# Performance work log

Measured on AMD Instinct MI355X. Metric: run time of the kernel, lower is better.

Reference implementation:

```python
import jax, jax.numpy as jnp
import numpy as np

HS = 512
IN = 512
FS = 128


def setup_inputs() -> dict:
    key = jax.random.key(0)
    ks = jax.random.split(key, 6)
    stdv = 1.0 / np.sqrt(HS)
    u = lambda k, shape: jax.random.uniform(k, shape, jnp.float32, -stdv, stdv)
    return {
        "word_input": jax.random.normal(ks[0], (128, 512, IN), jnp.float32),
        "field_input": jax.random.normal(ks[1], (128, 512, FS), jnp.float32),
        "W_f": u(ks[2], (IN, 4 * HS)),
        "Wz": u(ks[3], (FS, 2 * HS)),
        "U_f": u(ks[4], (HS, 4 * HS)),
        "bias_f": jnp.zeros((4 * HS,), jnp.float32),
        "biasz": jnp.zeros((2 * HS,), jnp.float32),
    }


def reference(word_input, field_input, W_f, Wz, U_f, bias_f, biasz):
    bs = word_input.shape[0]
    # Precompute input and field projections once (hoisted out of recurrence).
    x_proj = jnp.einsum("bsi,ih->bsh", word_input, W_f) + bias_f   # [B,S,4H]
    fgates = jnp.einsum("bsf,fh->bsh", field_input, Wz) + biasz     # [B,S,2H]
    lt = jax.nn.sigmoid(fgates[..., :HS])
    zt = jnp.tanh(fgates[..., HS:])
    lz = lt * zt                                                    # [B,S,H]

    h0 = jnp.zeros((bs, HS), jnp.float32)
    c0 = jnp.zeros((bs, HS), jnp.float32)

    def step(carry, inp):
        h_t, c_t = carry
        xp_t, lz_t = inp
        gates = xp_t + h_t @ U_f                     # [B,4H]
        i_t = jax.nn.sigmoid(gates[:, :HS])
        f_t = jax.nn.sigmoid(gates[:, HS:2 * HS] + 1.0)
        g_t = jnp.tanh(gates[:, 2 * HS:3 * HS])
        o_t = jax.nn.sigmoid(gates[:, 3 * HS:])
        c_t = f_t * c_t + i_t * g_t + lz_t
        h_t = o_t * jnp.tanh(c_t)
        return (h_t, c_t), h_t

    (h_T, c_T), hs = jax.lax.scan(
        step, (h0, c0),
        (jnp.swapaxes(x_proj, 0, 1), jnp.swapaxes(lz, 0, 1)))  # scan over seq
    hidden_seq = jnp.swapaxes(hs, 0, 1)  # [B,S,H]
    return hidden_seq, (h_T, c_T)
```

## Files before the change

kernel.cpp:

```cpp
#include <hip/hip_runtime.h>
#include <hip/hip_bf16.h>

#define BATCH 128
#define SEQ   512
#define IND   512
#define FSD   128
#define HS    512
#define G4    (4 * HS)
#define G2    (2 * HS)

#define NG 8
#define GB 16
#define NS 32
#define SJ 16

typedef short short8_t __attribute__((ext_vector_type(8)));
typedef float f32x4 __attribute__((ext_vector_type(4)));

static __device__ __forceinline__ unsigned short f2bf(float f) {
    unsigned int u = __float_as_uint(f);
    unsigned int r = (u + 0x7fffu + ((u >> 16) & 1u)) >> 16;
    return (unsigned short)r;
}
static __device__ __forceinline__ float bf2f(unsigned short b) {
    return __uint_as_float(((unsigned int)b) << 16);
}
static __device__ __forceinline__ float sigmoidf_(float x) {
    return 1.0f / (1.0f + __expf(-x));
}

__global__ __launch_bounds__(256)
void uconv_kernel(const float* __restrict__ Uf, unsigned short* __restrict__ Up) {
    int idx = blockIdx.x * 256 + threadIdx.x;
    int i  = idx & 7;
    int l  = (idx >> 3) & 63;
    int kt = (idx >> 9) & 15;
    int g  = (idx >> 13) & 3;
    int s  = idx >> 15;
    int k  = kt * 32 + ((l >> 4) << 3) + i;
    int col = g * 512 + s * 16 + (l & 15);
    Up[idx] = f2bf(Uf[(size_t)k * G4 + col]);
}

__global__ __launch_bounds__(256)
void wtconv_kernel(const float* __restrict__ Wf, unsigned short* __restrict__ WfT) {
    __shared__ float tile[64][65];
    int k0 = blockIdx.x * 64;
    int n0 = blockIdx.y * 64;
    int tid = threadIdx.x;
    int r = tid >> 6, c = tid & 63;
    #pragma unroll
    for (int i = 0; i < 16; ++i)
        tile[r + 4 * i][c] = Wf[(size_t)(k0 + r + 4 * i) * G4 + n0 + c];
    __syncthreads();
    #pragma unroll
    for (int i = 0; i < 16; ++i)
        WfT[(size_t)(n0 + r + 4 * i) * IND + k0 + c] = f2bf(tile[c][r + 4 * i]);
}

__global__ __launch_bounds__(256)
void wzconv_kernel(const float* __restrict__ Wz, unsigned short* __restrict__ WzT) {
    __shared__ float tile[64][65];
    int k0 = blockIdx.x * 64;
    int n0 = blockIdx.y * 64;
    int tid = threadIdx.x;
    int r = tid >> 6, c = tid & 63;
    #pragma unroll
    for (int i = 0; i < 16; ++i)
        tile[r + 4 * i][c] = Wz[(size_t)(k0 + r + 4 * i) * G2 + n0 + c];
    __syncthreads();
    #pragma unroll
    for (int i = 0; i < 16; ++i)
        WzT[(size_t)(n0 + r + 4 * i) * FSD + k0 + c] = f2bf(tile[c][r + 4 * i]);
}

__global__ __launch_bounds__(256)
void lzmm_kernel(const float* __restrict__ field, const unsigned short* __restrict__ WzT,
                 const float* __restrict__ biasz, unsigned short* __restrict__ lzOut) {
    __shared__ unsigned short As[128 * 64];
    __shared__ unsigned short Bs[128 * 64];
    int tid = threadIdx.x;
    int l = tid & 63, w = tid >> 6;
    int wr = w >> 1, wc = w & 1;
    int row0 = blockIdx.x * 128;
    int j0 = blockIdx.y * 64;

    f32x4 acc[4][4];
    #pragma unroll
    for (int m = 0; m < 4; ++m)
        #pragma unroll
        for (int n = 0; n < 4; ++n)
            acc[m][n] = (f32x4){0.f, 0.f, 0.f, 0.f};

    for (int k0 = 0; k0 < FSD; k0 += 64) {
        float4 av[4][2];
        short8_t bv[4];
        #pragma unroll
        for (int i = 0; i < 4; ++i) {
            int cidx = tid + 256 * i;
            int ar = cidx >> 3, sub = cidx & 7;
            int grow = row0 + ar;
            int b_ = grow & 127, s_ = grow >> 7;
            const float* ap = field + ((size_t)b_ * SEQ + s_) * FSD + k0 + sub * 8;
            av[i][0] = *(const float4*)ap;
            av[i][1] = *(const float4*)(ap + 4);
            int wzcol = ((ar >> 4) & 1) * HS + j0 + (((ar >> 5) << 4) | (ar & 15));
            bv[i] = *(const short8_t*)(WzT + (size_t)wzcol * FSD + k0 + sub * 8);
        }
        __syncthreads();
        #pragma unroll
        for (int i = 0; i < 4; ++i) {
            int cidx = tid + 256 * i;
            int ar = cidx >> 3, sub = cidx & 7;
            int off = ar * 64 + ((sub ^ (ar & 7)) << 3);
            short8_t a8;
            a8[0] = (short)f2bf(av[i][0].x); a8[1] = (short)f2bf(av[i][0].y);
            a8[2] = (short)f2bf(av[i][0].z); a8[3] = (short)f2bf(av[i][0].w);
            a8[4] = (short)f2bf(av[i][1].x); a8[5] = (short)f2bf(av[i][1].y);
            a8[6] = (short)f2bf(av[i][1].z); a8[7] = (short)f2bf(av[i][1].w);
            *(short8_t*)&As[off] = a8;
            *(short8_t*)&Bs[off] = bv[i];
        }
        __syncthreads();
        #pragma unroll
        for (int kt = 0; kt < 2; ++kt) {
            short8_t af[4], bfr[4];
            #pragma unroll
            for (int m = 0; m < 4; ++m) {
                int r = wr * 64 + m * 16 + (l & 15);
                int sub = kt * 4 + (l >> 4);
                af[m] = *(const short8_t*)&As[r * 64 + ((sub ^ (r & 7)) << 3)];
                int cc = wc * 64 + m * 16 + (l & 15);
                bfr[m] = *(const short8_t*)&Bs[cc * 64 + ((sub ^ (cc & 7)) << 3)];
            }
            #pragma unroll
            for (int m = 0; m < 4; ++m)
                #pragma unroll
                for (int n = 0; n < 4; ++n)
                    acc[m][n] = __builtin_amdgcn_mfma_f32_16x16x32_bf16(
                        af[m], bfr[n], acc[m][n], 0, 0, 0);
        }
        __syncthreads();
    }
    #pragma unroll
    for (int m = 0; m < 4; ++m) {
        int grow = row0 + wr * 64 + m * 16 + (l >> 4) * 4;
        #pragma unroll
        for (int q = 0; q < 2; ++q) {
            int j = j0 + (wc * 2 + q) * 16 + (l & 15);
            float bl = biasz[j];
            float bz = biasz[HS + j];
            f32x4 al = acc[m][2 * q];
            f32x4 az = acc[m][2 * q + 1];
            #pragma unroll
            for (int r = 0; r < 4; ++r) {
                float lv = sigmoidf_(al[r] + bl);
                float zv = tanhf(az[r] + bz);
                lzOut[(size_t)(grow + r) * HS + j] = f2bf(lv * zv);
            }
        }
    }
}

#define XBM 128
#define XBN 128
#define XBK 64
__global__ __launch_bounds__(256)
void xmm_kernel(const float* __restrict__ word, const unsigned short* __restrict__ WfT,
                const float* __restrict__ bias, unsigned short* __restrict__ xp) {
    __shared__ unsigned short As[XBM * XBK];
    __shared__ unsigned short Bs[XBN * XBK];
    int tid = threadIdx.x;
    int l = tid & 63, w = tid >> 6;
    int wr = w >> 1, wc = w & 1;
    int row0 = blockIdx.x * XBM;
    int col0 = blockIdx.y * XBN;

    f32x4 acc[4][4];
    #pragma unroll
    for (int m = 0; m < 4; ++m)
        #pragma unroll
        for (int n = 0; n < 4; ++n)
            acc[m][n] = (f32x4){0.f, 0.f, 0.f, 0.f};

    for (int k0 = 0; k0 < IND; k0 += XBK) {
        float4 av[4][2];
        short8_t bv[4];
        #pragma unroll
        for (int i = 0; i < 4; ++i) {
            int c = tid + 256 * i;
            int ar = c >> 3, sub = c & 7;
            int grow = row0 + ar;
            int b_ = grow & 127, s_ = grow >> 7;
            const float* ap = word + ((size_t)b_ * SEQ + s_) * IND + k0 + sub * 8;
            av[i][0] = *(const float4*)ap;
            av[i][1] = *(const float4*)(ap + 4);
            bv[i] = *(const short8_t*)(WfT + (size_t)(col0 + ar) * IND + k0 + sub * 8);
        }
        __syncthreads();
        #pragma unroll
        for (int i = 0; i < 4; ++i) {
            int c = tid + 256 * i;
            int ar = c >> 3, sub = c & 7;
            int off = ar * 64 + ((sub ^ (ar & 7)) << 3);
            short8_t a8;
            a8[0] = (short)f2bf(av[i][0].x); a8[1] = (short)f2bf(av[i][0].y);
            a8[2] = (short)f2bf(av[i][0].z); a8[3] = (short)f2bf(av[i][0].w);
            a8[4] = (short)f2bf(av[i][1].x); a8[5] = (short)f2bf(av[i][1].y);
            a8[6] = (short)f2bf(av[i][1].z); a8[7] = (short)f2bf(av[i][1].w);
            *(short8_t*)&As[off] = a8;
            *(short8_t*)&Bs[off] = bv[i];
        }
        __syncthreads();
        #pragma unroll
        for (int kt = 0; kt < 2; ++kt) {
            short8_t af[4], bfr[4];
            #pragma unroll
            for (int m = 0; m < 4; ++m) {
                int r = wr * 64 + m * 16 + (l & 15);
                int sub = kt * 4 + (l >> 4);
                af[m] = *(const short8_t*)&As[r * 64 + ((sub ^ (r & 7)) << 3)];
                int cc = wc * 64 + m * 16 + (l & 15);
                bfr[m] = *(const short8_t*)&Bs[cc * 64 + ((sub ^ (cc & 7)) << 3)];
            }
            #pragma unroll
            for (int m = 0; m < 4; ++m)
                #pragma unroll
                for (int n = 0; n < 4; ++n)
                    acc[m][n] = __builtin_amdgcn_mfma_f32_16x16x32_bf16(
                        af[m], bfr[n], acc[m][n], 0, 0, 0);
        }
    }
    #pragma unroll
    for (int m = 0; m < 4; ++m) {
        int grow = row0 + wr * 64 + m * 16 + (l >> 4) * 4;
        #pragma unroll
        for (int n = 0; n < 4; ++n) {
            int gcol = col0 + wc * 64 + n * 16 + (l & 15);
            float bsv = bias[gcol];
            #pragma unroll
            for (int r = 0; r < 4; ++r)
                xp[(size_t)(grow + r) * G4 + gcol] = f2bf(acc[m][n][r] + bsv);
        }
    }
}

__global__ __launch_bounds__(256, 1)
void rec12_kernel(const unsigned short* __restrict__ xp,
                  const unsigned short* __restrict__ lz,
                  const unsigned short* __restrict__ Up,
                  float* __restrict__ out,
                  unsigned short* __restrict__ hbuf,
                  unsigned int* __restrict__ flags) {
    const size_t HSEQ = (size_t)BATCH * SEQ * HS;
    const int HBG = GB * HS;

    int bid = blockIdx.x;
    int g = bid & 7;
    int s = bid >> 3;
    int tid = threadIdx.x;
    int w = tid >> 6;
    int l = tid & 63;

    __shared__ short8_t Ubs[4][16][64];
    {
        const short8_t* upw = (const short8_t*)(Up + ((size_t)(s * 4 + w) * 16) * 512);
        #pragma unroll
        for (int kt = 0; kt < 16; ++kt)
            Ubs[w][kt][l] = upw[kt * 64 + l];
    }
    __shared__ short8_t ha_lds[16][64];
    __shared__ float gbuf[4][16][18];
    __syncthreads();

    int eb = tid >> 4;
    int ej = tid & 15;
    int jg = s * SJ + ej;
    int bg = g * GB + eb;
    int widx = (((jg >> 5) * 64 + eb + (((jg >> 3) & 3) << 4)) << 3) + (jg & 7);

    unsigned int* fl = flags + (size_t)g * 2 * NS;

    float c = 0.f, h_last = 0.f;

    for (int t = 0; t < SEQ; ++t) {
        size_t xb = ((size_t)t * BATCH + bg) * G4;
        float pgi = bf2f(xp[xb + jg]);
        float pgf = bf2f(xp[xb + HS + jg]);
        float pgg = bf2f(xp[xb + 2 * HS + jg]);
        float pgo = bf2f(xp[xb + 3 * HS + jg]);
        float plz = bf2f(lz[((size_t)t * BATCH + bg) * HS + jg]);

        f32x4 acc0 = {0.f, 0.f, 0.f, 0.f};
        f32x4 acc1 = {0.f, 0.f, 0.f, 0.f};
        if (t > 0) {
            if (w == 0) {
                const unsigned int* fp = fl + ((t - 1) & 1) * NS + (l & 31);
                int spins = 0;
                unsigned v;
                do {
                    v = __hip_atomic_load(fp, __ATOMIC_RELAXED,
                                          __HIP_MEMORY_SCOPE_AGENT);
                    if (++spins > (1 << 20)) break;
                } while (!__all(v == (unsigned)t));

                const unsigned long long* ha64 = (const unsigned long long*)
                    (hbuf + (size_t)(((t - 1) & 1) * NG + g) * HBG);
                unsigned long long A2a[16], A2b[16];
                #pragma unroll
                for (int kt = 0; kt < 16; ++kt) {
                    int i0 = (kt * 64 + l) * 2;
                    A2a[kt] = __hip_atomic_load(&ha64[i0], __ATOMIC_RELAXED,
                                                __HIP_MEMORY_SCOPE_AGENT);
                    A2b[kt] = __hip_atomic_load(&ha64[i0 + 1], __ATOMIC_RELAXED,
                                                __HIP_MEMORY_SCOPE_AGENT);
                }
                #pragma unroll
                for (int kt = 0; kt < 16; ++kt) {
                    union { unsigned long long u[2]; short8_t v8; } A;
                    A.u[0] = A2a[kt]; A.u[1] = A2b[kt];
                    ha_lds[kt][l] = A.v8;
                }
            }
            __syncthreads();

            #pragma unroll
            for (int kt = 0; kt < 16; ++kt) {
                short8_t av = ha_lds[kt][l];
                short8_t bf = Ubs[w][kt][l];
                if (kt & 1)
                    acc1 = __builtin_amdgcn_mfma_f32_16x16x32_bf16(av, bf, acc1, 0, 0, 0);
                else
                    acc0 = __builtin_amdgcn_mfma_f32_16x16x32_bf16(av, bf, acc0, 0, 0, 0);
            }
            acc0 += acc1;
        }
        #pragma unroll
        for (int r = 0; r < 4; ++r)
            gbuf[w][(l >> 4) * 4 + r][l & 15] = acc0[r];
        __syncthreads();

        float gi = gbuf[0][eb][ej] + pgi;
        float gf = gbuf[1][eb][ej] + pgf;
        float gg = gbuf[2][eb][ej] + pgg;
        float go = gbuf[3][eb][ej] + pgo;
        float i_ = sigmoidf_(gi);
        float f_ = sigmoidf_(gf + 1.0f);
        float g_ = tanhf(gg);
        float o_ = sigmoidf_(go);
        c = f_ * c + i_ * g_ + plz;
        float h = o_ * tanhf(c);
        h_last = h;

        unsigned short hv = f2bf(h);
        unsigned partner = (unsigned)(unsigned short)__shfl_down((int)hv, 1);
        if ((ej & 1) == 0) {
            unsigned int* hb32 = (unsigned int*)
                (hbuf + (size_t)((t & 1) * NG + g) * HBG);
            __hip_atomic_store(&hb32[widx >> 1], (unsigned)hv | (partner << 16),
                               __ATOMIC_RELAXED, __HIP_MEMORY_SCOPE_AGENT);
        }
        asm volatile("s_waitcnt vmcnt(0)" ::: "memory");
        __syncthreads();
        if (tid == 0)
            __hip_atomic_store(&fl[(t & 1) * NS + s], (unsigned)(t + 1),
                               __ATOMIC_RELAXED, __HIP_MEMORY_SCOPE_AGENT);

        out[((size_t)bg * SEQ + t) * HS + jg] = h;
    }

    out[HSEQ + (size_t)bg * HS + jg] = h_last;
    out[HSEQ + (size_t)BATCH * HS + (size_t)bg * HS + jg] = c;
}

extern "C" void kernel_launch(void* const* d_in, const int* in_sizes, int n_in,
                              void* d_out, int out_size, void* d_ws, size_t ws_size,
                              hipStream_t stream) {
    const float* word   = (const float*)d_in[0];
    const float* field  = (const float*)d_in[1];
    const float* Wf     = (const float*)d_in[2];
    const float* Wz     = (const float*)d_in[3];
    const float* Uf     = (const float*)d_in[4];
    const float* bias_f = (const float*)d_in[5];
    const float* biasz  = (const float*)d_in[6];
    float* out = (float*)d_out;

    char* p = (char*)d_ws;
    unsigned short* xp   = (unsigned short*)p;  p += (size_t)SEQ * BATCH * G4 * 2;
    unsigned short* lzb  = (unsigned short*)p;  p += (size_t)SEQ * BATCH * HS * 2;
    unsigned short* Up   = (unsigned short*)p;  p += (size_t)IND * G4 * 2;
    unsigned short* WfT  = (unsigned short*)p;  p += (size_t)G4 * IND * 2;
    unsigned short* WzT  = (unsigned short*)p;  p += (size_t)G2 * FSD * 2;
    unsigned short* hbuf = (unsigned short*)p;  p += (size_t)2 * NG * GB * HS * 2;
    unsigned int*   flags= (unsigned int*)p;    p += (size_t)NG * 2 * NS * 4;

    hipMemsetAsync(flags, 0, (size_t)NG * 2 * NS * 4, stream);

    uconv_kernel<<<(IND * G4) / 256, 256, 0, stream>>>(Uf, Up);

    dim3 gt(IND / 64, G4 / 64);
    wtconv_kernel<<<gt, 256, 0, stream>>>(Wf, WfT);

    dim3 gz(FSD / 64, G2 / 64);
    wzconv_kernel<<<gz, 256, 0, stream>>>(Wz, WzT);

    dim3 glz((SEQ * BATCH) / 128, HS / 64);
    lzmm_kernel<<<glz, 256, 0, stream>>>(field, WzT, biasz, lzb);

    dim3 gx((SEQ * BATCH) / XBM, G4 / XBN);
    xmm_kernel<<<gx, 256, 0, stream>>>(word, WfT, bias_f, xp);

    rec12_kernel<<<NG * NS, 256, 0, stream>>>(xp, lzb, Up, out, hbuf, flags);
}
```

Measured before the change: 1.803 ms.

## Halve recurrence workgroups with 32 hidden units each; swizzle GEMM grid per XCD

The recurrent kernel now launches 128 workgroups instead of 256. Each handles 32 hidden columns, with two U-slices held in LDS and two MFMA chains per wave, and each thread updates two batch rows. This halves the number of participants in the per-step flag barrier and the spinning on flags, but doubles the serial MFMA and elementwise work per workgroup on every step. Separately, the input-projection GEMM switches to a 1D grid remapped so that each XCD gets a contiguous band of rows, which is meant to improve L2 locality.

```diff
diff --git a/kernel.cpp b/kernel.cpp
--- a/kernel.cpp
+++ b/kernel.cpp
@@ -11,8 +11,8 @@
 
 #define NG 8
 #define GB 16
-#define NS 32
-#define SJ 16
+#define NB2 16
+#define SJ2 32
 
 typedef short short8_t __attribute__((ext_vector_type(8)));
 typedef float f32x4 __attribute__((ext_vector_type(4)));
@@ -173,8 +173,11 @@
     int tid = threadIdx.x;
     int l = tid & 63, w = tid >> 6;
     int wr = w >> 1, wc = w & 1;
-    int row0 = blockIdx.x * XBM;
-    int col0 = blockIdx.y * XBN;
+    int lin = blockIdx.x;
+    int xcd = lin & 7;
+    int idx = lin >> 3;
+    int col0 = (idx & 15) * XBN;
+    int row0 = (xcd * 64 + (idx >> 4)) * XBM;
 
     f32x4 acc[4][4];
     #pragma unroll
@@ -246,7 +249,7 @@
 }
 
 __global__ __launch_bounds__(256, 1)
-void rec12_kernel(const unsigned short* __restrict__ xp,
+void rec13_kernel(const unsigned short* __restrict__ xp,
                   const unsigned short* __restrict__ lz,
                   const unsigned short* __restrict__ Up,
                   float* __restrict__ out,
@@ -262,40 +265,50 @@
     int w = tid >> 6;
     int l = tid & 63;
 
-    __shared__ short8_t Ubs[4][16][64];
-    {
-        const short8_t* upw = (const short8_t*)(Up + ((size_t)(s * 4 + w) * 16) * 512);
+    __shared__ short8_t Ubs[2][4][16][64];
+    #pragma unroll
+    for (int sl = 0; sl < 2; ++sl) {
+        const short8_t* upw =
+            (const short8_t*)(Up + ((size_t)((2 * s + sl) * 4 + w) * 16) * 512);
         #pragma unroll
         for (int kt = 0; kt < 16; ++kt)
-            Ubs[w][kt][l] = upw[kt * 64 + l];
+            Ubs[sl][w][kt][l] = upw[kt * 64 + l];
     }
     __shared__ short8_t ha_lds[16][64];
-    __shared__ float gbuf[4][16][18];
+    __shared__ float gbuf[4][16][34];
     __syncthreads();
 
-    int eb = tid >> 4;
-    int ej = tid & 15;
-    int jg = s * SJ + ej;
-    int bg = g * GB + eb;
-    int widx = (((jg >> 5) * 64 + eb + (((jg >> 3) & 3) << 4)) << 3) + (jg & 7);
-
-    unsigned int* fl = flags + (size_t)g * 2 * NS;
-
-    float c = 0.f, h_last = 0.f;
+    int ej = tid & 31;
+    int eb0 = tid >> 5;
+    int jg = s * SJ2 + ej;
+    int bg0 = g * GB + eb0;
+    int bg1 = bg0 + 8;
+    int w0 = (((jg >> 5) * 64 + eb0 + (((jg >> 3) & 3) << 4)) << 3) + (jg & 7);
+    int w1 = w0 + 64;
+
+    unsigned int* fl = flags + (size_t)g * 2 * NB2;
+
+    float c0 = 0.f, c1 = 0.f, h0l = 0.f, h1l = 0.f;
 
     for (int t = 0; t < SEQ; ++t) {
-        size_t xb = ((size_t)t * BATCH + bg) * G4;
-        float pgi = bf2f(xp[xb + jg]);
-        float pgf = bf2f(xp[xb + HS + jg]);
-        float pgg = bf2f(xp[xb + 2 * HS + jg]);
-        float pgo = bf2f(xp[xb + 3 * HS + jg]);
-        float plz = bf2f(lz[((size_t)t * BATCH + bg) * HS + jg]);
-
-        f32x4 acc0 = {0.f, 0.f, 0.f, 0.f};
-        f32x4 acc1 = {0.f, 0.f, 0.f, 0.f};
+        size_t xb0 = ((size_t)t * BATCH + bg0) * G4;
+        size_t xb1 = ((size_t)t * BATCH + bg1) * G4;
+        float pgi0 = bf2f(xp[xb0 + jg]);
+        float pgf0 = bf2f(xp[xb0 + HS + jg]);
+        float pgg0 = bf2f(xp[xb0 + 2 * HS + jg]);
+        float pgo0 = bf2f(xp[xb0 + 3 * HS + jg]);
+        float pgi1 = bf2f(xp[xb1 + jg]);
+        float pgf1 = bf2f(xp[xb1 + HS + jg]);
+        float pgg1 = bf2f(xp[xb1 + 2 * HS + jg]);
+        float pgo1 = bf2f(xp[xb1 + 3 * HS + jg]);
+        float plz0 = bf2f(lz[((size_t)t * BATCH + bg0) * HS + jg]);
+        float plz1 = bf2f(lz[((size_t)t * BATCH + bg1) * HS + jg]);
+
+        f32x4 aA0 = {0.f,0.f,0.f,0.f}, aA1 = {0.f,0.f,0.f,0.f};
+        f32x4 aB0 = {0.f,0.f,0.f,0.f}, aB1 = {0.f,0.f,0.f,0.f};
         if (t > 0) {
             if (w == 0) {
-                const unsigned int* fp = fl + ((t - 1) & 1) * NS + (l & 31);
+                const unsigned int* fp = fl + ((t - 1) & 1) * NB2 + (l & 15);
                 int spins = 0;
                 unsigned v;
                 do {
@@ -327,50 +340,69 @@
             #pragma unroll
             for (int kt = 0; kt < 16; ++kt) {
                 short8_t av = ha_lds[kt][l];
-                short8_t bf = Ubs[w][kt][l];
-                if (kt & 1)
-                    acc1 = __builtin_amdgcn_mfma_f32_16x16x32_bf16(av, bf, acc1, 0, 0, 0);
-                else
-                    acc0 = __builtin_amdgcn_mfma_f32_16x16x32_bf16(av, bf, acc0, 0, 0, 0);
+                short8_t bfA = Ubs[0][w][kt][l];
+                short8_t bfB = Ubs[1][w][kt][l];
+                if (kt & 1) {
+                    aA1 = __builtin_amdgcn_mfma_f32_16x16x32_bf16(av, bfA, aA1, 0, 0, 0);
+                    aB1 = __builtin_amdgcn_mfma_f32_16x16x32_bf16(av, bfB, aB1, 0, 0, 0);
+                } else {
+                    aA0 = __builtin_amdgcn_mfma_f32_16x16x32_bf16(av, bfA, aA0, 0, 0, 0);
+                    aB0 = __builtin_amdgcn_mfma_f32_16x16x32_bf16(av, bfB, aB0, 0, 0, 0);
+                }
             }
-            acc0 += acc1;
-        }
-        #pragma unroll
-        for (int r = 0; r < 4; ++r)
-            gbuf[w][(l >> 4) * 4 + r][l & 15] = acc0[r];
-        __syncthreads();
-
-        float gi = gbuf[0][eb][ej] + pgi;
-        float gf = gbuf[1][eb][ej] + pgf;
-        float gg = gbuf[2][eb][ej] + pgg;
-        float go = gbuf[3][eb][ej] + pgo;
-        float i_ = sigmoidf_(gi);
-        float f_ = sigmoidf_(gf + 1.0f);
-        float g_ = tanhf(gg);
-        float o_ = sigmoidf_(go);
-        c = f_ * c + i_ * g_ + plz;
-        float h = o_ * tanhf(c);
-        h_last = h;
-
-        unsigned short hv = f2bf(h);
-        unsigned partner = (unsigned)(unsigned short)__shfl_down((int)hv, 1);
+            aA0 += aA1;
+            aB0 += aB1;
+        }
+        #pragma unroll
+        for (int r = 0; r < 4; ++r) {
+            gbuf[w][(l >> 4) * 4 + r][l & 15] = aA0[r];
+            gbuf[w][(l >> 4) * 4 + r][16 + (l & 15)] = aB0[r];
+        }
+        __syncthreads();
+
+        float gi0 = gbuf[0][eb0][ej] + pgi0;
+        float gf0 = gbuf[1][eb0][ej] + pgf0;
+        float gg0 = gbuf[2][eb0][ej] + pgg0;
+        float go0 = gbuf[3][eb0][ej] + pgo0;
+        float gi1 = gbuf[0][eb0 + 8][ej] + pgi1;
+        float gf1 = gbuf[1][eb0 + 8][ej] + pgf1;
+        float gg1 = gbuf[2][eb0 + 8][ej] + pgg1;
+        float go1 = gbuf[3][eb0 + 8][ej] + pgo1;
+        float i0 = sigmoidf_(gi0), f0 = sigmoidf_(gf0 + 1.0f);
+        float q0 = tanhf(gg0),     o0 = sigmoidf_(go0);
+        float i1 = sigmoidf_(gi1), f1 = sigmoidf_(gf1 + 1.0f);
+        float q1 = tanhf(gg1),     o1 = sigmoidf_(go1);
+        c0 = f0 * c0 + i0 * q0 + plz0;
+        c1 = f1 * c1 + i1 * q1 + plz1;
+        float h0 = o0 * tanhf(c0);
+        float h1 = o1 * tanhf(c1);
+        h0l = h0; h1l = h1;
+
+        unsigned short hv0 = f2bf(h0), hv1 = f2bf(h1);
+        unsigned p0 = (unsigned)(unsigned short)__shfl_down((int)hv0, 1);
+        unsigned p1 = (unsigned)(unsigned short)__shfl_down((int)hv1, 1);
         if ((ej & 1) == 0) {
             unsigned int* hb32 = (unsigned int*)
                 (hbuf + (size_t)((t & 1) * NG + g) * HBG);
-            __hip_atomic_store(&hb32[widx >> 1], (unsigned)hv | (partner << 16),
+            __hip_atomic_store(&hb32[w0 >> 1], (unsigned)hv0 | (p0 << 16),
                                __ATOMIC_RELAXED, __HIP_MEMORY_SCOPE_AGENT);
+            __hip_atomic_store(&hb32[w1 >> 1], (unsigned)hv1 | (p1 << 16),
+                               __ATOMIC_RELAXED, __HIP_MEMORY_SCOPE_AGENT);
         }
         asm volatile("s_waitcnt vmcnt(0)" ::: "memory");
         __syncthreads();
         if (tid == 0)
-            __hip_atomic_store(&fl[(t & 1) * NS + s], (unsigned)(t + 1),
+            __hip_atomic_store(&fl[(t & 1) * NB2 + s], (unsigned)(t + 1),
                                __ATOMIC_RELAXED, __HIP_MEMORY_SCOPE_AGENT);
 
-        out[((size_t)bg * SEQ + t) * HS + jg] = h;
-    }
-
-    out[HSEQ + (size_t)bg * HS + jg] = h_last;
-    out[HSEQ + (size_t)BATCH * HS + (size_t)bg * HS + jg] = c;
+        out[((size_t)bg0 * SEQ + t) * HS + jg] = h0;
+        out[((size_t)bg1 * SEQ + t) * HS + jg] = h1;
+    }
+
+    out[HSEQ + (size_t)bg0 * HS + jg] = h0l;
+    out[HSEQ + (size_t)bg1 * HS + jg] = h1l;
+    out[HSEQ + (size_t)BATCH * HS + (size_t)bg0 * HS + jg] = c0;
+    out[HSEQ + (size_t)BATCH * HS + (size_t)bg1 * HS + jg] = c1;
 }
 
 extern "C" void kernel_launch(void* const* d_in, const int* in_sizes, int n_in,
@@ -392,9 +424,9 @@
     unsigned short* WfT  = (unsigned short*)p;  p += (size_t)G4 * IND * 2;
     unsigned short* WzT  = (unsigned short*)p;  p += (size_t)G2 * FSD * 2;
     unsigned short* hbuf = (unsigned short*)p;  p += (size_t)2 * NG * GB * HS * 2;
-    unsigned int*   flags= (unsigned int*)p;    p += (size_t)NG * 2 * NS * 4;
-
-    hipMemsetAsync(flags, 0, (size_t)NG * 2 * NS * 4, stream);
+    unsigned int*   flags= (unsigned int*)p;    p += 2048;
+
+    hipMemsetAsync(flags, 0, 2048, stream);
 
     uconv_kernel<<<(IND * G4) / 256, 256, 0, stream>>>(Uf, Up);
 
@@ -407,8 +439,8 @@
     dim3 glz((SEQ * BATCH) / 128, HS / 64);
     lzmm_kernel<<<glz, 256, 0, stream>>>(field, WzT, biasz, lzb);
 
-    dim3 gx((SEQ * BATCH) / XBM, G4 / XBN);
-    xmm_kernel<<<gx, 256, 0, stream>>>(word, WfT, bias_f, xp);
-
-    rec12_kernel<<<NG * NS, 256, 0, stream>>>(xp, lzb, Up, out, hbuf, flags);
-}
+    xmm_kernel<<<(SEQ * BATCH / XBM) * (G4 / XBN), 256, 0, stream>>>(
+        word, WfT, bias_f, xp);
+
+    rec13_kernel<<<NG * NB2, 256, 0, stream>>>(xp, lzb, Up, out, hbuf, flags);
+}
```

Result: slower. 1.962 ms (+8.8%).

## Tag hidden-state words with timestep to replace flag barrier in recurrence

Applied to the files above, without the earlier changes.

The recurrent kernel no longer uses separate per-block flags with a store/waitcnt/syncthreads/flag-store handshake. Each h value is stored as a 32-bit word holding the bf16 value plus a timestep tag, and consumers spin directly on the data until every tag matches, with all four waves polling in parallel instead of one. This removes a barrier and a round trip per step on the critical serial path, at the cost of doubling hbuf traffic and adding tag checks. Separately, the input-projection GEMM grid is linearised and remapped so blocks sharing rows land on the same XCD, aiming for better L2 reuse.

```diff
diff --git a/kernel.cpp b/kernel.cpp
--- a/kernel.cpp
+++ b/kernel.cpp
@@ -173,8 +173,11 @@
     int tid = threadIdx.x;
     int l = tid & 63, w = tid >> 6;
     int wr = w >> 1, wc = w & 1;
-    int row0 = blockIdx.x * XBM;
-    int col0 = blockIdx.y * XBN;
+    int lin = blockIdx.x;
+    int xcd = lin & 7;
+    int idx = lin >> 3;
+    int col0 = (idx & 15) * XBN;
+    int row0 = (xcd * 64 + (idx >> 4)) * XBM;
 
     f32x4 acc[4][4];
     #pragma unroll
@@ -246,12 +249,11 @@
 }
 
 __global__ __launch_bounds__(256, 1)
-void rec12_kernel(const unsigned short* __restrict__ xp,
+void rec14_kernel(const unsigned short* __restrict__ xp,
                   const unsigned short* __restrict__ lz,
                   const unsigned short* __restrict__ Up,
                   float* __restrict__ out,
-                  unsigned short* __restrict__ hbuf,
-                  unsigned int* __restrict__ flags) {
+                  unsigned int* __restrict__ hbuf) {
     const size_t HSEQ = (size_t)BATCH * SEQ * HS;
     const int HBG = GB * HS;
 
@@ -278,8 +280,6 @@
     int jg = s * SJ + ej;
     int bg = g * GB + eb;
     int widx = (((jg >> 5) * 64 + eb + (((jg >> 3) & 3) << 4)) << 3) + (jg & 7);
-
-    unsigned int* fl = flags + (size_t)g * 2 * NS;
 
     float c = 0.f, h_last = 0.f;
 
@@ -294,33 +294,41 @@
         f32x4 acc0 = {0.f, 0.f, 0.f, 0.f};
         f32x4 acc1 = {0.f, 0.f, 0.f, 0.f};
         if (t > 0) {
-            if (w == 0) {
-                const unsigned int* fp = fl + ((t - 1) & 1) * NS + (l & 31);
+            unsigned expect = (unsigned)t;
+            const unsigned long long* ha64 = (const unsigned long long*)
+                (hbuf + (size_t)(((t - 1) & 1) * NG + g) * HBG);
+            #pragma unroll
+            for (int q = 0; q < 4; ++q) {
+                int kt = w * 4 + q;
+                const unsigned long long* pk = ha64 + (size_t)kt * 256 + l * 4;
+                unsigned long long x0, x1, x2, x3;
                 int spins = 0;
-                unsigned v;
-                do {
-                    v = __hip_atomic_load(fp, __ATOMIC_RELAXED,
-                                          __HIP_MEMORY_SCOPE_AGENT);
-                    if (++spins > (1 << 20)) break;
-                } while (!__all(v == (unsigned)t));
-
-                const unsigned long long* ha64 = (const unsigned long long*)
-                    (hbuf + (size_t)(((t - 1) & 1) * NG + g) * HBG);
-                unsigned long long A2a[16], A2b[16];
-                #pragma unroll
-                for (int kt = 0; kt < 16; ++kt) {
-                    int i0 = (kt * 64 + l) * 2;
-                    A2a[kt] = __hip_atomic_load(&ha64[i0], __ATOMIC_RELAXED,
-                                                __HIP_MEMORY_SCOPE_AGENT);
-                    A2b[kt] = __hip_atomic_load(&ha64[i0 + 1], __ATOMIC_RELAXED,
-                                                __HIP_MEMORY_SCOPE_AGENT);
+                for (;;) {
+                    x0 = __hip_atomic_load(pk + 0, __ATOMIC_RELAXED,
+                                           __HIP_MEMORY_SCOPE_AGENT);
+                    x1 = __hip_atomic_load(pk + 1, __ATOMIC_RELAXED,
+                                           __HIP_MEMORY_SCOPE_AGENT);
+                    x2 = __hip_atomic_load(pk + 2, __ATOMIC_RELAXED,
+                                           __HIP_MEMORY_SCOPE_AGENT);
+                    x3 = __hip_atomic_load(pk + 3, __ATOMIC_RELAXED,
+                                           __HIP_MEMORY_SCOPE_AGENT);
+                    bool ok =
+                        (((unsigned)(x0 >> 16) & 0xffffu) == expect) &
+                        (((unsigned)(x0 >> 48)) == expect) &
+                        (((unsigned)(x1 >> 16) & 0xffffu) == expect) &
+                        (((unsigned)(x1 >> 48)) == expect) &
+                        (((unsigned)(x2 >> 16) & 0xffffu) == expect) &
+                        (((unsigned)(x2 >> 48)) == expect) &
+                        (((unsigned)(x3 >> 16) & 0xffffu) == expect) &
+                        (((unsigned)(x3 >> 48)) == expect);
+                    if (__all(ok) || ++spins > (1 << 20)) break;
                 }
-                #pragma unroll
-                for (int kt = 0; kt < 16; ++kt) {
-                    union { unsigned long long u[2]; short8_t v8; } A;
-                    A.u[0] = A2a[kt]; A.u[1] = A2b[kt];
-                    ha_lds[kt][l] = A.v8;
-                }
+                union { unsigned int u[4]; short8_t v8; } A;
+                A.u[0] = __builtin_amdgcn_perm((unsigned)(x0 >> 32), (unsigned)x0, 0x05040100u);
+                A.u[1] = __builtin_amdgcn_perm((unsigned)(x1 >> 32), (unsigned)x1, 0x05040100u);
+                A.u[2] = __builtin_amdgcn_perm((unsigned)(x2 >> 32), (unsigned)x2, 0x05040100u);
+                A.u[3] = __builtin_amdgcn_perm((unsigned)(x3 >> 32), (unsigned)x3, 0x05040100u);
+                ha_lds[kt][l] = A.v8;
             }
             __syncthreads();
 
@@ -352,19 +360,10 @@
         float h = o_ * tanhf(c);
         h_last = h;
 
-        unsigned short hv = f2bf(h);
-        unsigned partner = (unsigned)(unsigned short)__shfl_down((int)hv, 1);
-        if ((ej & 1) == 0) {
-            unsigned int* hb32 = (unsigned int*)
-                (hbuf + (size_t)((t & 1) * NG + g) * HBG);
-            __hip_atomic_store(&hb32[widx >> 1], (unsigned)hv | (partner << 16),
-                               __ATOMIC_RELAXED, __HIP_MEMORY_SCOPE_AGENT);
-        }
-        asm volatile("s_waitcnt vmcnt(0)" ::: "memory");
-        __syncthreads();
-        if (tid == 0)
-            __hip_atomic_store(&fl[(t & 1) * NS + s], (unsigned)(t + 1),
-                               __ATOMIC_RELAXED, __HIP_MEMORY_SCOPE_AGENT);
+        unsigned tagval = (unsigned)f2bf(h) | ((unsigned)(t + 1) << 16);
+        unsigned int* hb = hbuf + (size_t)((t & 1) * NG + g) * HBG;
+        __hip_atomic_store(&hb[widx], tagval, __ATOMIC_RELAXED,
+                           __HIP_MEMORY_SCOPE_AGENT);
 
         out[((size_t)bg * SEQ + t) * HS + jg] = h;
     }
@@ -391,10 +390,9 @@
     unsigned short* Up   = (unsigned short*)p;  p += (size_t)IND * G4 * 2;
     unsigned short* WfT  = (unsigned short*)p;  p += (size_t)G4 * IND * 2;
     unsigned short* WzT  = (unsigned short*)p;  p += (size_t)G2 * FSD * 2;
-    unsigned short* hbuf = (unsigned short*)p;  p += (size_t)2 * NG * GB * HS * 2;
-    unsigned int*   flags= (unsigned int*)p;    p += (size_t)NG * 2 * NS * 4;
-
-    hipMemsetAsync(flags, 0, (size_t)NG * 2 * NS * 4, stream);
+    unsigned int*   hbuf = (unsigned int*)p;    p += (size_t)2 * NG * GB * HS * 4;
+
+    hipMemsetAsync(hbuf, 0, (size_t)2 * NG * GB * HS * 4, stream);
 
     uconv_kernel<<<(IND * G4) / 256, 256, 0, stream>>>(Uf, Up);
 
@@ -407,8 +405,8 @@
     dim3 glz((SEQ * BATCH) / 128, HS / 64);
     lzmm_kernel<<<glz, 256, 0, stream>>>(field, WzT, biasz, lzb);
 
-    dim3 gx((SEQ * BATCH) / XBM, G4 / XBN);
-    xmm_kernel<<<gx, 256, 0, stream>>>(word, WfT, bias_f, xp);
-
-    rec12_kernel<<<NG * NS, 256, 0, stream>>>(xp, lzb, Up, out, hbuf, flags);
-}
+    xmm_kernel<<<(SEQ * BATCH / XBM) * (G4 / XBN), 256, 0, stream>>>(
+        word, WfT, bias_f, xp);
+
+    rec14_kernel<<<NG * NS, 256, 0, stream>>>(xp, lzb, Up, out, hbuf);
+}
```

Result: slower. 2.319 ms (+28.6%).

## Use per-wave completion flags in recurrence and XCD-swizzle the input GEMM grid

Applied to the files above, without the earlier changes.

The recurrent kernel drops the block-wide barrier before publishing step completion; each wave now writes its own flag, and waiters poll four times as many flags with two loads per lane. The input-projection GEMM switches to a 1D grid remapped so that blocks on the same XCD share row tiles, improving L2 reuse. The per-wave flags shorten the critical path per timestep but raise polling traffic.

```diff
diff --git a/kernel.cpp b/kernel.cpp
--- a/kernel.cpp
+++ b/kernel.cpp
@@ -173,8 +173,11 @@
     int tid = threadIdx.x;
     int l = tid & 63, w = tid >> 6;
     int wr = w >> 1, wc = w & 1;
-    int row0 = blockIdx.x * XBM;
-    int col0 = blockIdx.y * XBN;
+    int lin = blockIdx.x;
+    int xcd = lin & 7;
+    int idx = lin >> 3;
+    int col0 = (idx & 15) * XBN;
+    int row0 = (xcd * 64 + (idx >> 4)) * XBM;
 
     f32x4 acc[4][4];
     #pragma unroll
@@ -246,7 +249,7 @@
 }
 
 __global__ __launch_bounds__(256, 1)
-void rec12_kernel(const unsigned short* __restrict__ xp,
+void rec15_kernel(const unsigned short* __restrict__ xp,
                   const unsigned short* __restrict__ lz,
                   const unsigned short* __restrict__ Up,
                   float* __restrict__ out,
@@ -279,7 +282,7 @@
     int bg = g * GB + eb;
     int widx = (((jg >> 5) * 64 + eb + (((jg >> 3) & 3) << 4)) << 3) + (jg & 7);
 
-    unsigned int* fl = flags + (size_t)g * 2 * NS;
+    unsigned int* fl = flags + (size_t)g * 2 * NS * 4;
 
     float c = 0.f, h_last = 0.f;
 
@@ -295,14 +298,18 @@
         f32x4 acc1 = {0.f, 0.f, 0.f, 0.f};
         if (t > 0) {
             if (w == 0) {
-                const unsigned int* fp = fl + ((t - 1) & 1) * NS + (l & 31);
+                const unsigned int* fb = fl + ((t - 1) & 1) * NS * 4;
+                const unsigned int* fp0 = fb + l;
+                const unsigned int* fp1 = fb + 64 + l;
                 int spins = 0;
-                unsigned v;
+                unsigned v0, v1;
                 do {
-                    v = __hip_atomic_load(fp, __ATOMIC_RELAXED,
-                                          __HIP_MEMORY_SCOPE_AGENT);
+                    v0 = __hip_atomic_load(fp0, __ATOMIC_RELAXED,
+                                           __HIP_MEMORY_SCOPE_AGENT);
+                    v1 = __hip_atomic_load(fp1, __ATOMIC_RELAXED,
+                                           __HIP_MEMORY_SCOPE_AGENT);
                     if (++spins > (1 << 20)) break;
-                } while (!__all(v == (unsigned)t));
+                } while (!__all((v0 == (unsigned)t) & (v1 == (unsigned)t)));
 
                 const unsigned long long* ha64 = (const unsigned long long*)
                     (hbuf + (size_t)(((t - 1) & 1) * NG + g) * HBG);
@@ -361,9 +368,9 @@
                                __ATOMIC_RELAXED, __HIP_MEMORY_SCOPE_AGENT);
         }
         asm volatile("s_waitcnt vmcnt(0)" ::: "memory");
-        __syncthreads();
-        if (tid == 0)
-            __hip_atomic_store(&fl[(t & 1) * NS + s], (unsigned)(t + 1),
+        if (l == 0)
+            __hip_atomic_store(&fl[(t & 1) * NS * 4 + s * 4 + w],
+                               (unsigned)(t + 1),
                                __ATOMIC_RELAXED, __HIP_MEMORY_SCOPE_AGENT);
 
         out[((size_t)bg * SEQ + t) * HS + jg] = h;
@@ -392,9 +399,9 @@
     unsigned short* WfT  = (unsigned short*)p;  p += (size_t)G4 * IND * 2;
     unsigned short* WzT  = (unsigned short*)p;  p += (size_t)G2 * FSD * 2;
     unsigned short* hbuf = (unsigned short*)p;  p += (size_t)2 * NG * GB * HS * 2;
-    unsigned int*   flags= (unsigned int*)p;    p += (size_t)NG * 2 * NS * 4;
-
-    hipMemsetAsync(flags, 0, (size_t)NG * 2 * NS * 4, stream);
+    unsigned int*   flags= (unsigned int*)p;    p += (size_t)NG * 2 * NS * 4 * 4;
+
+    hipMemsetAsync(flags, 0, (size_t)NG * 2 * NS * 4 * 4, stream);
 
     uconv_kernel<<<(IND * G4) / 256, 256, 0, stream>>>(Uf, Up);
 
@@ -407,8 +414,8 @@
     dim3 glz((SEQ * BATCH) / 128, HS / 64);
     lzmm_kernel<<<glz, 256, 0, stream>>>(field, WzT, biasz, lzb);
 
-    dim3 gx((SEQ * BATCH) / XBM, G4 / XBN);
-    xmm_kernel<<<gx, 256, 0, stream>>>(word, WfT, bias_f, xp);
-
-    rec12_kernel<<<NG * NS, 256, 0, stream>>>(xp, lzb, Up, out, hbuf, flags);
-}
+    xmm_kernel<<<(SEQ * BATCH / XBM) * (G4 / XBN), 256, 0, stream>>>(
+        word, WfT, bias_f, xp);
+
+    rec15_kernel<<<NG * NS, 256, 0, stream>>>(xp, lzb, Up, out, hbuf, flags);
+}
```

Result: slower. 3.048 ms (+69.1%).
